# Optimization experiments

Measured on AMD Instinct MI355X. Metric: run time of the kernel, lower is better.

## Reference

```python
import jax, jax.numpy as jnp
import numpy as np

N_HEADS = 8
EPS = 1e-8


def _build_gp_map():
    # Cl(4,1) geometric-product structure constants. Blade index = 5-bit mask,
    # e1..e5 = bits 0..4; metric (+,+,+,+,-): e5 (bit 4) squares to -1.
    def pc(n):
        return bin(n).count("1")
    g = np.zeros((32, 32, 32), np.float32)
    for a in range(32):
        for b in range(32):
            swaps = 0
            aa = a >> 1
            while aa:
                swaps += pc(aa & b)
                aa >>= 1
            sign = -1.0 if (swaps & 1) else 1.0
            if (a & b) & 0b10000:  # shared e5 factor contributes -1
                sign = -sign
            g[a, b, a ^ b] = sign
    return g

GP_MAP = jnp.asarray(_build_gp_map())          # (32,32,32)
BIVEC_IDX = jnp.array([3, 5, 6, 9, 10, 12, 17, 18, 20, 24])  # grade-2 blades
SCALAR_VECTOR_IDX = np.array([0, 1, 2, 4, 8, 16])            # grade-0 + grade-1


def normalize_cl41(x):
    return x / jnp.sqrt(jnp.sum(x * x, axis=-1, keepdims=True) + EPS)


def geometric_linear(w, x):
    # w: (O,I,32), x: (...,I,32) -> (...,O,32)
    wg = jnp.einsum('oij,jlk->oilk', w, GP_MAP)     # fold gp_map into weight
    out = jnp.einsum('oilk,...il->...ok', wg, x)
    return normalize_cl41(out)


def _init_weight(key, out_f, in_f):
    # Grade-aware Xavier: only scalar + vector lanes are nonzero.
    std = 1.0 / np.sqrt(in_f * 32)
    vals = jax.random.normal(key, (out_f, in_f, len(SCALAR_VECTOR_IDX)), jnp.float32) * std
    w = jnp.zeros((out_f, in_f, 32), jnp.float32)
    return w.at[:, :, SCALAR_VECTOR_IDX].set(vals)


def setup_inputs() -> dict:
    key = jax.random.key(0)
    kx, kq, kk, kv, ko = jax.random.split(key, 5)
    B, S, D = 2, 384, 128
    x = jax.random.normal(kx, (B, S, D, 32), jnp.float32)
    return {
        'x': x,
        'wq': _init_weight(kq, D, D),
        'wk': _init_weight(kk, D, D),
        'wv': _init_weight(kv, D, D),
        'wo': _init_weight(ko, D, D),
        'attn_lambda': jnp.float32(0.1),
    }


def reference(x, wq, wk, wv, wo, attn_lambda):
    B, S, D, _ = x.shape
    H = N_HEADS
    hd = D // H
    def split_heads(t):  # (B,S,D,32) -> (B,H,S,hd,32)
        return t.reshape(B, S, H, hd, 32).transpose(0, 2, 1, 3, 4)
    q = split_heads(geometric_linear(wq, x))
    k = split_heads(geometric_linear(wk, x))
    v = split_heads(geometric_linear(wv, x))

    # Geometric product Q*K contracted over head_dim, then over gp_map lanes.
    qg = jnp.einsum('bhsdi,ijk->bhsdjk', q, GP_MAP)      # (B,H,S,hd,32,32)
    raw_mv = jnp.einsum('bhsdjk,bhxdj->bhsxk', qg, k)    # (B,H,S,S,32)
    raw_mv = normalize_cl41(raw_mv)

    scalar_part = raw_mv[..., 0]
    biv = raw_mv[..., BIVEC_IDX]
    bivector_norm = jnp.sqrt(jnp.sum(biv * biv, axis=-1) + EPS)
    score = (scalar_part + attn_lambda * bivector_norm) / np.sqrt(hd).astype(np.float32)
    attn_probs = jax.nn.softmax(score, axis=-1)          # (B,H,S,S)

    out = jnp.einsum('bhsx,bhxdl->bhsdl', attn_probs, v)  # (B,H,S,hd,32)
    out = out.transpose(0, 2, 1, 3, 4).reshape(B, S, D, 32)
    return geometric_linear(wo, out)
```

## Files before the change

### kernel.cpp

```cpp
#include <hip/hip_runtime.h>
#include <math.h>

#define BB    2
#define SS    384
#define DD    128
#define NH    8
#define HDIM  16
#define NBH   16
#define BS    768

typedef unsigned int   u32;
typedef unsigned short u16;
typedef __attribute__((ext_vector_type(8))) short short8;
typedef __attribute__((ext_vector_type(4))) float f32x4;

struct SignTab { float v[32][32]; };
constexpr int popcnt32c(int x){ int c=0; for(int i=0;i<32;i++) c += (x>>i)&1; return c; }
constexpr int signgp_int(int a, int b){
  int swaps=0; int aa=a>>1;
  while(aa){ swaps += popcnt32c(aa & b); aa >>= 1; }
  int s = (swaps & 1) ? -1 : 1;
  if ((a & b) & 16) s = -s;
  return s;
}
constexpr SignTab make_signs(){
  SignTab t{};
  for(int a=0;a<32;a++) for(int b=0;b<32;b++)
    t.v[a][b] = (float)signgp_int(a,b);
  return t;
}
constexpr SignTab GPS = make_signs();

struct MaskTab { u32 v[4][8][4][4]; };
constexpr MaskTab mkmask(){
  MaskTab t{};
  for(int w=0;w<4;w++) for(int u=0;u<8;u++) for(int q=0;q<4;q++) for(int r=0;r<4;r++){
    u32 m = 0;
    for(int h=0;h<2;h++){
      int j = 2*r + h;
      int i = (q<<3) | j;
      int c = (w<<3) | u;
      if (signgp_int(i, i^c) < 0) m |= (h ? 0x80000000u : 0x8000u);
    }
    t.v[w][u][q][r] = m;
  }
  return t;
}
constexpr MaskTab MT = mkmask();

__device__ __forceinline__ u16 f2bf(float f){
  u32 x = __float_as_uint(f);
  return (u16)((x + 0x7FFFu + ((x>>16)&1u)) >> 16);
}
__device__ __forceinline__ float bf2f(u16 h){
  return __uint_as_float(((u32)h) << 16);
}

#define XLS 33
__global__ __launch_bounds__(256) void gather_k(const float* __restrict__ src,
                                                u16* __restrict__ xg,
                                                const float* __restrict__ wq,
                                                const float* __restrict__ wk,
                                                const float* __restrict__ wv,
                                                const float* __restrict__ wo,
                                                u16* __restrict__ wpk2){
  if (blockIdx.y == 1){
    int idx = blockIdx.x*256 + threadIdx.x;
    int o   = idx / 768;
    int rem = idx - o*768;
    int jp  = rem >> 7;
    int i   = rem & 127;
    const int SV[6] = {0,1,2,4,8,16};
    const float* ww[4] = {wq, wk, wv, wo};
    #pragma unroll
    for(int p=0;p<4;p++)
      wpk2[p*98304 + idx] = f2bf(ww[p][(o*128 + i)*32 + SV[jp]]);
    return;
  }

  __shared__ float xl[2*128*XLS];
  int t = threadIdx.x;
  int bs0 = blockIdx.x*2;
  int bsl = t >> 7, i = t & 127;

  float row[32];
  const float4* s4 = (const float4*)(src + (((size_t)(bs0+bsl)*128 + i)*32));
  #pragma unroll
  for(int r=0;r<8;r++){
    float4 v = s4[r];
    row[r*4+0]=v.x; row[r*4+1]=v.y; row[r*4+2]=v.z; row[r*4+3]=v.w;
  }
  float* xrow = xl + bsl*128*XLS + i*XLS;
  #pragma unroll
  for(int l=0;l<32;l++) xrow[l] = row[l];
  __syncthreads();

  const int SV[6] = {0,1,2,4,8,16};
  u32* xg32 = (u32*)xg;
  #pragma unroll 4
  for(int r=0;r<96;r++){
    int wr = t + r*256;
    int k   = wr / 768;
    int rem = wr - k*768;
    int bl  = rem / 384;
    int r2  = rem - bl*384;
    int jp  = r2 >> 6;
    int ip  = r2 & 63;
    int i2  = ip*2;
    int b   = SV[jp] ^ k;
    float sg = GPS.v[SV[jp]][b];
    const float* base = xl + bl*128*XLS;
    float f0 = base[ i2   *XLS + b] * sg;
    float f1 = base[(i2+1)*XLS + b] * sg;
    u32 pk = (u32)f2bf(f0) | ((u32)f2bf(f1) << 16);
    xg32[((size_t)k*768 + bs0 + bl)*384 + jp*64 + ip] = pk;
  }
}

#define LSTR 40
__global__ __launch_bounds__(256) void gemm_proj(const u16* __restrict__ xg,
                                                 const u16* __restrict__ wpkA,
                                                 u16* __restrict__ tmpA){
  __shared__ __align__(16) u16 As[128*LSTR];
  __shared__ __align__(16) u16 Bs[128*LSTR];
  int t = threadIdx.x;
  int Mt = blockIdx.x, k = blockIdx.y, p = blockIdx.z;
  const u16* wpk = wpkA + (size_t)p*98304;
  u16* tmp = tmpA + (size_t)p*32*768*128;

  int w = t >> 6, lane = t & 63;
  int q = lane >> 4, n16 = lane & 15;
  int wm = w >> 1, wn = w & 1;

  f32x4 acc[4][4];
  #pragma unroll
  for(int a=0;a<4;a++)
    #pragma unroll
    for(int b=0;b<4;b++) acc[a][b] = (f32x4){0.f,0.f,0.f,0.f};

  int r0 = t>>2, c0 = (t&3)*8;
  int r1 = (t+256)>>2, c1 = ((t+256)&3)*8;
  const u16* Aab = xg + ((size_t)k*768 + Mt*128)*768;

  uint4 pa0, pa1, pb0, pb1;
  {
    pa0 = *(const uint4*)(Aab + (size_t)r0*768 + c0);
    pa1 = *(const uint4*)(Aab + (size_t)r1*768 + c1);
    pb0 = *(const uint4*)(wpk + (size_t)r0*768 + c0);
    pb1 = *(const uint4*)(wpk + (size_t)r1*768 + c1);
  }

  for(int kt=0; kt<24; kt++){
    __syncthreads();
    *(uint4*)(As + r0*LSTR + c0) = pa0;
    *(uint4*)(As + r1*LSTR + c1) = pa1;
    *(uint4*)(Bs + r0*LSTR + c0) = pb0;
    *(uint4*)(Bs + r1*LSTR + c1) = pb1;
    __syncthreads();
    if (kt < 23){
      int kn = (kt+1)*32;
      pa0 = *(const uint4*)(Aab + (size_t)r0*768 + kn + c0);
      pa1 = *(const uint4*)(Aab + (size_t)r1*768 + kn + c1);
      pb0 = *(const uint4*)(wpk + (size_t)r0*768 + kn + c0);
      pb1 = *(const uint4*)(wpk + (size_t)r1*768 + kn + c1);
    }
    short8 a[4], b[4];
    #pragma unroll
    for(int mi=0;mi<4;mi++)
      a[mi] = *(const short8*)(As + (wm*64 + mi*16 + n16)*LSTR + q*8);
    #pragma unroll
    for(int ni=0;ni<4;ni++)
      b[ni] = *(const short8*)(Bs + (wn*64 + ni*16 + n16)*LSTR + q*8);
    #pragma unroll
    for(int mi=0;mi<4;mi++)
      #pragma unroll
      for(int ni=0;ni<4;ni++)
        acc[mi][ni] = __builtin_amdgcn_mfma_f32_16x16x32_bf16(a[mi], b[ni], acc[mi][ni], 0,0,0);
  }

  #pragma unroll
  for(int mi=0;mi<4;mi++){
    #pragma unroll
    for(int r=0;r<4;r++){
      int m = Mt*128 + wm*64 + mi*16 + q*4 + r;
      #pragma unroll
      for(int ni=0;ni<4;ni++){
        int n = wn*64 + ni*16 + n16;
        tmp[((size_t)k*768 + m)*128 + n] = f2bf(acc[mi][ni][r]);
      }
    }
  }
}

__global__ __launch_bounds__(256) void norm3(const u16* __restrict__ tmpA,
                                             u16* __restrict__ qhb,
                                             u16* __restrict__ khb,
                                             u16* __restrict__ vbb){
  int z = blockIdx.y;
  const u16* tmp = tmpA + (size_t)z*32*768*128;
  u16* dst = (z==0)?qhb:(z==1)?khb:vbb;
  int t = threadIdx.x;
  int bsl = t >> 7, o = t & 127;
  int bs = blockIdx.x*2 + bsl;

  float a[32];
  float ssum = 1e-8f;
  #pragma unroll
  for(int k=0;k<32;k++){
    a[k] = bf2f(tmp[((size_t)k*768 + bs)*128 + o]);
    ssum = fmaf(a[k], a[k], ssum);
  }
  float inv = 1.0f / sqrtf(ssum);

  int b = bs / SS, s = bs - b*SS;
  int h = o >> 4, d = o & 15;
  uint4* og4 = (uint4*)(dst + (((size_t)(b*NH + h)*SS + s)*512 + d*32));
  #pragma unroll
  for(int l=0;l<4;l++){
    uint4 v;
    v.x = (u32)f2bf(a[8*l+0]*inv) | ((u32)f2bf(a[8*l+1]*inv)<<16);
    v.y = (u32)f2bf(a[8*l+2]*inv) | ((u32)f2bf(a[8*l+3]*inv)<<16);
    v.z = (u32)f2bf(a[8*l+4]*inv) | ((u32)f2bf(a[8*l+5]*inv)<<16);
    v.w = (u32)f2bf(a[8*l+6]*inv) | ((u32)f2bf(a[8*l+7]*inv)<<16);
    og4[l] = v;
  }
}

__global__ __launch_bounds__(256) void norm_out(const u16* __restrict__ tmp,
                                                float* __restrict__ dst){
  int t = threadIdx.x;
  int bsl = t >> 7, o = t & 127;
  int bs = blockIdx.x*2 + bsl;

  float a[32];
  float ssum = 1e-8f;
  #pragma unroll
  for(int k=0;k<32;k++){
    a[k] = bf2f(tmp[((size_t)k*768 + bs)*128 + o]);
    ssum = fmaf(a[k], a[k], ssum);
  }
  float inv = 1.0f / sqrtf(ssum);
  float4* og = (float4*)(dst + ((size_t)bs*128 + o)*32);
  #pragma unroll
  for(int l4=0;l4<8;l4++){
    float4 v;
    v.x = a[4*l4+0]*inv; v.y = a[4*l4+1]*inv;
    v.z = a[4*l4+2]*inv; v.w = a[4*l4+3]*inv;
    og[l4] = v;
  }
}

#define TVS 528
__global__ __launch_bounds__(256) void transpose_v(const u16* __restrict__ vb,
                                                   u16* __restrict__ vt){
  __shared__ __align__(16) u16 vl[32*TVS];
  int t = threadIdx.x;
  int xt = blockIdx.x, bh = blockIdx.y;
  const u16* src = vb + ((size_t)bh*SS + xt*32)*512;
  #pragma unroll
  for(int j=0;j<8;j++){
    int f = t + j*256; int row = f>>6, c = (f&63)*8;
    *(uint4*)(vl + row*TVS + c) = *(const uint4*)(src + (size_t)row*512 + c);
  }
  __syncthreads();
  u16* dst = vt + (size_t)bh*512*SS + xt*32;
  #pragma unroll
  for(int j=0;j<8;j++){
    int f = t + j*256; int dl = f>>2, c4 = (f&3)*8;
    u16 tmp[8];
    #pragma unroll
    for(int e=0;e<8;e++) tmp[e] = vl[(c4+e)*TVS + dl];
    *(uint4*)(dst + (size_t)dl*SS + c4) = *(uint4*)tmp;
  }
}

#define QSTR 264
__global__ __launch_bounds__(256,2) void scores_mfma(const u16* __restrict__ qh,
                                                     const u16* __restrict__ kh,
                                                     float* __restrict__ sc,
                                                     const float* __restrict__ lam){
  __shared__ __align__(16) u16 smem[(64+16)*QSTR];
  u16* qs = smem;
  u16* ks = smem + 64*QSTR;
  int t = threadIdx.x;
  int id  = blockIdx.x;
  int xcd = id & 7;
  int g   = id >> 3;
  int half= g / 144;
  int r9  = g - half*144;
  int bh  = xcd + 8*half;
  int st  = r9 / 24;
  int xt  = r9 - st*24;

  int w = t >> 6, lane = t & 63, q = lane >> 4, mn = lane & 15;
  float lm = lam[0];

  u32 FM[8][4];
  #pragma unroll
  for(int u=0;u<8;u++)
    #pragma unroll
    for(int r=0;r<4;r++) FM[u][r] = MT.v[w][u][q][r];

  f32x4 acc[4][8];
  #pragma unroll
  for(int mi=0;mi<4;mi++)
    #pragma unroll
    for(int u=0;u<8;u++) acc[mi][u] = (f32x4){0.f,0.f,0.f,0.f};

  for(int h=0; h<2; h++){
    __syncthreads();
    const u16* qbase = qh + ((size_t)bh*SS + st*64)*512 + h*256;
    const u16* kbase = kh + ((size_t)bh*SS + xt*16)*512 + h*256;
    #pragma unroll
    for(int j=0;j<8;j++){
      int f = t + j*256;
      int row = f>>5, c = (f&31)*8;
      *(uint4*)(qs + row*QSTR + c) = *(const uint4*)(qbase + (size_t)row*512 + c);
    }
    #pragma unroll
    for(int j=0;j<2;j++){
      int f = t + j*256;
      int row = f>>5, c = (f&31)*8;
      *(uint4*)(ks + row*QSTR + c) = *(const uint4*)(kbase + (size_t)row*512 + c);
    }
    __syncthreads();

    for(int ktl=0; ktl<8; ktl++){
      short8 a[4];
      #pragma unroll
      for(int mi=0;mi<4;mi++)
        a[mi] = *(const short8*)(qs + (mi*16+mn)*QSTR + ktl*32 + q*8);
      uint4 khd = *(const uint4*)(ks + mn*QSTR + ktl*32 + ((q^w)<<3));
      u32 kk[4]  = {khd.x, khd.y, khd.z, khd.w};
      u32 kks[4];
      #pragma unroll
      for(int r=0;r<4;r++) kks[r] = (kk[r]>>16)|(kk[r]<<16);
      #pragma unroll
      for(int u=0;u<8;u++){
        union { u32 w32[4]; short8 s; } bf;
        #pragma unroll
        for(int r=0;r<4;r++){
          u32 v = (u & 1) ? kks[r ^ (u>>1)] : kk[r ^ (u>>1)];
          bf.w32[r] = v ^ FM[u][r];
        }
        #pragma unroll
        for(int mi=0;mi<4;mi++)
          acc[mi][u] = __builtin_amdgcn_mfma_f32_16x16x32_bf16(a[mi], bf.s, acc[mi][u], 0, 0, 0);
      }
    }
  }
  __syncthreads();

  float* pss = (float*)smem;
  float* pbb = pss + 64*68;
  float* ps0 = pbb + 64*68;

  #pragma unroll
  for(int mi=0;mi<4;mi++){
    #pragma unroll
    for(int rr=0;rr<4;rr++){
      float ssv = 0.f, bbv = 0.f;
      #pragma unroll
      for(int u=0;u<8;u++){
        int c = w*8 + u;
        bool isb = (c==3)||(c==5)||(c==6)||(c==9)||(c==10)||(c==12)||
                   (c==17)||(c==18)||(c==20)||(c==24);
        float v = acc[mi][u][rr];
        ssv = fmaf(v, v, ssv);
        if (isb) bbv = fmaf(v, v, bbv);
      }
      int s = mi*16 + q*4 + rr;
      pss[s*68 + w*16 + mn] = ssv;
      pbb[s*68 + w*16 + mn] = bbv;
      if (w == 0) ps0[s*17 + mn] = acc[mi][0][rr];
    }
  }
  __syncthreads();

  int x = t & 15, s0 = t >> 4;
  #pragma unroll
  for(int ssi=0; ssi<4; ssi++){
    int s = s0 + ssi*16;
    float ss = 1e-8f, bb = 0.f;
    #pragma unroll
    for(int ww=0; ww<4; ww++){
      ss += pss[s*68 + ww*16 + x];
      bb += pbb[s*68 + ww*16 + x];
    }
    float inv = 1.0f / sqrtf(ss);
    float s0v = ps0[s*17+x];
    float score = (s0v*inv + lm*sqrtf(bb*inv*inv + 1e-8f)) * 0.25f;
    sc[((size_t)bh*SS + st*64 + s)*SS + xt*16 + x] = score;
  }
}

#define PBS 392
#define VSS 40
__global__ __launch_bounds__(256,2) void pv_mfma(const float* __restrict__ sc,
                                                 const u16* __restrict__ vt,
                                                 u32* __restrict__ xgo){
  __shared__ __align__(16) u16 pb[16*PBS];
  __shared__ __align__(16) u16 vsm[512*VSS];
  int t = threadIdx.x;
  int id  = blockIdx.x;
  int xcd = id & 7;
  int g   = id >> 3;
  int half= g / 24;
  int st  = g - half*24;
  int bh  = xcd + 8*half;
  int w = t >> 6, lane = t & 63, q = lane >> 4, mn = lane & 15;

  {
    int row = t >> 4, gg = t & 15;
    const float* srow = sc + ((size_t)bh*SS + st*16 + row)*SS;
    float v[24];
    float mx = -1e30f;
    #pragma unroll
    for(int k2=0;k2<24;k2++){ v[k2] = srow[gg + k2*16]; mx = fmaxf(mx, v[k2]); }
    #pragma unroll
    for(int off=8; off; off>>=1) mx = fmaxf(mx, __shfl_xor(mx, off));
    float sum = 0.f;
    #pragma unroll
    for(int k2=0;k2<24;k2++){ v[k2] = __expf(v[k2]-mx); sum += v[k2]; }
    #pragma unroll
    for(int off=8; off; off>>=1) sum += __shfl_xor(sum, off);
    float inv = 1.f/sum;
    #pragma unroll
    for(int k2=0;k2<24;k2++) pb[row*PBS + gg + k2*16] = f2bf(v[k2]*inv);
  }

  f32x4 acc[8];
  #pragma unroll
  for(int mt=0;mt<8;mt++) acc[mt] = (f32x4){0.f,0.f,0.f,0.f};

  const u16* vtb = vt + (size_t)bh*512*SS;
  for(int kt=0; kt<12; kt++){
    __syncthreads();
    #pragma unroll
    for(int j=0;j<8;j++){
      int f = t + j*256;
      int dl = f>>2, c4 = (f&3)*8;
      *(uint4*)(vsm + dl*VSS + c4) = *(const uint4*)(vtb + (size_t)dl*SS + kt*32 + c4);
    }
    __syncthreads();
    short8 b = *(const short8*)(pb + mn*PBS + kt*32 + q*8);
    #pragma unroll
    for(int mt=0;mt<8;mt++){
      short8 a = *(const short8*)(vsm + ((w*8+mt)*16 + mn)*VSS + q*8);
      acc[mt] = __builtin_amdgcn_mfma_f32_16x16x32_bf16(a, b, acc[mt], 0, 0, 0);
    }
  }
  __syncthreads();

  float* ot = (float*)vsm;
  #pragma unroll
  for(int mt=0;mt<8;mt++)
    #pragma unroll
    for(int rr=0;rr<4;rr++){
      int dl = (w*8+mt)*16 + q*4 + rr;
      int row = ((dl & 31) << 4) | (dl >> 5);
      ot[row*17 + mn] = acc[mt][rr];
    }
  __syncthreads();

  int b = bh >> 3, h = bh & 7;
  int bs_base = b*SS + st*16;
  const int SVc[6] = {0,1,2,4,8,16};
  #pragma unroll 4
  for(int it=0; it<96; it++){
    int idx = it*256 + t;
    int dp = idx & 7;
    int s  = (idx >> 3) & 15;
    int jl = idx >> 7;
    int jp = jl >> 5;
    int l  = jl & 31;
    int k  = SVc[jp] ^ l;
    float sg = GPS.v[SVc[jp]][l];
    float v0 = sg * ot[(l*16 + dp*2    )*17 + s];
    float v1 = sg * ot[(l*16 + dp*2 + 1)*17 + s];
    u32 pk = (u32)f2bf(v0) | ((u32)f2bf(v1) << 16);
    xgo[((size_t)k*768 + bs_base + s)*384 + (size_t)(jp*64 + h*8 + dp)] = pk;
  }
}

extern "C" void kernel_launch(void* const* d_in, const int* in_sizes, int n_in,
                              void* d_out, int out_size, void* d_ws, size_t ws_size,
                              hipStream_t stream) {
  const float* x   = (const float*)d_in[0];
  const float* wq  = (const float*)d_in[1];
  const float* wk  = (const float*)d_in[2];
  const float* wv  = (const float*)d_in[3];
  const float* wo  = (const float*)d_in[4];
  const float* lam = (const float*)d_in[5];
  float* out = (float*)d_out;

  char* ws = (char*)d_ws;
  size_t off = 0;
  u16*   wpk2 = (u16*)(ws + off); off += (size_t)4*98304*2;
  u16*   xg   = (u16*)(ws + off); off += (size_t)32*768*768*2;
  u16*   tmp3 = (u16*)(ws + off); off += (size_t)3*32*768*128*2;
  u16*   vt   = tmp3;
  float* sc   = (float*)((char*)tmp3 + 6291456);
  u16*   qhb  = (u16*)(ws + off); off += (size_t)NBH*SS*512*2;
  u16*   khb  = (u16*)(ws + off); off += (size_t)NBH*SS*512*2;
  u16*   vb   = (u16*)(ws + off); off += (size_t)NBH*SS*512*2;

  gather_k<<<dim3(384,2),256,0,stream>>>(x, xg, wq, wk, wv, wo, wpk2);
  gemm_proj<<<dim3(6,32,3),256,0,stream>>>(xg, wpk2, tmp3);
  norm3<<<dim3(384,3),256,0,stream>>>(tmp3, qhb, khb, vb);
  transpose_v<<<dim3(12,16),256,0,stream>>>(vb, vt);

  scores_mfma<<<2304,256,0,stream>>>(qhb, khb, sc, lam);
  pv_mfma<<<384,256,0,stream>>>(sc, vt, (u32*)xg);

  gemm_proj<<<dim3(6,32,1),256,0,stream>>>(xg, wpk2 + (size_t)3*98304, tmp3);
  norm_out<<<384,256,0,stream>>>(tmp3, out);
}
```

Before: 254.5 us.

## Split PV kernel over value halves and stagger per-block K-tile order

The PV kernel now launches twice as many blocks, each handling half of the 512 value columns, so shared memory and accumulator registers per block shrink and more blocks can fill the GPU. The softmax for each row is recomputed by both halves. Both the scores and PV kernels rotate the order in which they walk K tiles and head halves, using a hash of the block id, to spread concurrent memory accesses across channels. The cost is duplicated softmax work and extra index arithmetic.

```diff
diff --git a/kernel.cpp b/kernel.cpp
--- a/kernel.cpp
+++ b/kernel.cpp
@@ -292,6 +292,10 @@
   int st  = r9 / 24;
   int xt  = r9 - st*24;
 
+  u32 hsh  = (u32)id * 0x9E3779B9u;
+  int rot  = (int)(hsh >> 29);
+  int hrot = (int)(hsh >> 28) & 1;
+
   int w = t >> 6, lane = t & 63, q = lane >> 4, mn = lane & 15;
   float lm = lam[0];
 
@@ -307,7 +311,8 @@
     #pragma unroll
     for(int u=0;u<8;u++) acc[mi][u] = (f32x4){0.f,0.f,0.f,0.f};
 
-  for(int h=0; h<2; h++){
+  for(int hi=0; hi<2; hi++){
+    int h = hi ^ hrot;
     __syncthreads();
     const u16* qbase = qh + ((size_t)bh*SS + st*64)*512 + h*256;
     const u16* kbase = kh + ((size_t)bh*SS + xt*16)*512 + h*256;
@@ -326,11 +331,12 @@
     __syncthreads();
 
     for(int ktl=0; ktl<8; ktl++){
+      int ke = (ktl + rot) & 7;
       short8 a[4];
       #pragma unroll
       for(int mi=0;mi<4;mi++)
-        a[mi] = *(const short8*)(qs + (mi*16+mn)*QSTR + ktl*32 + q*8);
-      uint4 khd = *(const uint4*)(ks + mn*QSTR + ktl*32 + ((q^w)<<3));
+        a[mi] = *(const short8*)(qs + (mi*16+mn)*QSTR + ke*32 + q*8);
+      uint4 khd = *(const uint4*)(ks + mn*QSTR + ke*32 + ((q^w)<<3));
       u32 kk[4]  = {khd.x, khd.y, khd.z, khd.w};
       u32 kks[4];
       #pragma unroll
@@ -400,15 +406,20 @@
                                                  const u16* __restrict__ vt,
                                                  u32* __restrict__ xgo){
   __shared__ __align__(16) u16 pb[16*PBS];
-  __shared__ __align__(16) u16 vsm[512*VSS];
+  __shared__ __align__(16) u16 vsm[256*VSS];
   int t = threadIdx.x;
   int id  = blockIdx.x;
   int xcd = id & 7;
-  int g   = id >> 3;
-  int half= g / 24;
-  int st  = g - half*24;
+  int rest= id >> 3;
+  int z   = rest & 1;
+  int g2  = rest >> 1;
+  int half= g2 / 24;
+  int st  = g2 - half*24;
   int bh  = xcd + 8*half;
   int w = t >> 6, lane = t & 63, q = lane >> 4, mn = lane & 15;
+
+  u32 hsh = (u32)id * 0x9E3779B9u;
+  int rotp = (int)(hsh >> 30) * 3;
 
   {
     int row = t >> 4, gg = t & 15;
@@ -429,24 +440,25 @@
     for(int k2=0;k2<24;k2++) pb[row*PBS + gg + k2*16] = f2bf(v[k2]*inv);
   }
 
-  f32x4 acc[8];
-  #pragma unroll
-  for(int mt=0;mt<8;mt++) acc[mt] = (f32x4){0.f,0.f,0.f,0.f};
-
-  const u16* vtb = vt + (size_t)bh*512*SS;
+  f32x4 acc[4];
+  #pragma unroll
+  for(int mt=0;mt<4;mt++) acc[mt] = (f32x4){0.f,0.f,0.f,0.f};
+
+  const u16* vtb = vt + (size_t)bh*512*SS + (size_t)z*256*SS;
   for(int kt=0; kt<12; kt++){
+    int ke = kt + rotp; if (ke >= 12) ke -= 12;
     __syncthreads();
     #pragma unroll
-    for(int j=0;j<8;j++){
+    for(int j=0;j<4;j++){
       int f = t + j*256;
       int dl = f>>2, c4 = (f&3)*8;
-      *(uint4*)(vsm + dl*VSS + c4) = *(const uint4*)(vtb + (size_t)dl*SS + kt*32 + c4);
+      *(uint4*)(vsm + dl*VSS + c4) = *(const uint4*)(vtb + (size_t)dl*SS + ke*32 + c4);
     }
     __syncthreads();
-    short8 b = *(const short8*)(pb + mn*PBS + kt*32 + q*8);
-    #pragma unroll
-    for(int mt=0;mt<8;mt++){
-      short8 a = *(const short8*)(vsm + ((w*8+mt)*16 + mn)*VSS + q*8);
+    short8 b = *(const short8*)(pb + mn*PBS + ke*32 + q*8);
+    #pragma unroll
+    for(int mt=0;mt<4;mt++){
+      short8 a = *(const short8*)(vsm + ((w*4+mt)*16 + mn)*VSS + q*8);
       acc[mt] = __builtin_amdgcn_mfma_f32_16x16x32_bf16(a, b, acc[mt], 0, 0, 0);
     }
   }
@@ -454,11 +466,11 @@
 
   float* ot = (float*)vsm;
   #pragma unroll
-  for(int mt=0;mt<8;mt++)
+  for(int mt=0;mt<4;mt++)
     #pragma unroll
     for(int rr=0;rr<4;rr++){
-      int dl = (w*8+mt)*16 + q*4 + rr;
-      int row = ((dl & 31) << 4) | (dl >> 5);
+      int dl = (w*4+mt)*16 + q*4 + rr;
+      int row = ((dl & 31) << 3) | (dl >> 5);
       ot[row*17 + mn] = acc[mt][rr];
     }
   __syncthreads();
@@ -467,19 +479,19 @@
   int bs_base = b*SS + st*16;
   const int SVc[6] = {0,1,2,4,8,16};
   #pragma unroll 4
-  for(int it=0; it<96; it++){
+  for(int it=0; it<48; it++){
     int idx = it*256 + t;
-    int dp = idx & 7;
-    int s  = (idx >> 3) & 15;
-    int jl = idx >> 7;
-    int jp = jl >> 5;
-    int l  = jl & 31;
-    int k  = SVc[jp] ^ l;
+    int dpl = idx & 3;
+    int s   = (idx >> 2) & 15;
+    int jl  = idx >> 6;
+    int jp  = jl >> 5;
+    int l   = jl & 31;
+    int k   = SVc[jp] ^ l;
     float sg = GPS.v[SVc[jp]][l];
-    float v0 = sg * ot[(l*16 + dp*2    )*17 + s];
-    float v1 = sg * ot[(l*16 + dp*2 + 1)*17 + s];
+    float v0 = sg * ot[(l*8 + dpl*2    )*17 + s];
+    float v1 = sg * ot[(l*8 + dpl*2 + 1)*17 + s];
     u32 pk = (u32)f2bf(v0) | ((u32)f2bf(v1) << 16);
-    xgo[((size_t)k*768 + bs_base + s)*384 + (size_t)(jp*64 + h*8 + dp)] = pk;
+    xgo[((size_t)k*768 + bs_base + s)*384 + (size_t)(jp*64 + h*8 + z*4 + dpl)] = pk;
   }
 }
 
@@ -511,7 +523,7 @@
   transpose_v<<<dim3(12,16),256,0,stream>>>(vb, vt);
 
   scores_mfma<<<2304,256,0,stream>>>(qhb, khb, sc, lam);
-  pv_mfma<<<384,256,0,stream>>>(sc, vt, (u32*)xg);
+  pv_mfma<<<768,256,0,stream>>>(sc, vt, (u32*)xg);
 
   gemm_proj<<<dim3(6,32,1),256,0,stream>>>(xg, wpk2 + (size_t)3*98304, tmp3);
   norm_out<<<384,256,0,stream>>>(tmp3, out);
```

Result: no change. 256.5 us (+0.8%).
